# Optimization experiments

Measured on AMD Instinct MI355X. Metric: run time of the kernel, lower is better.

Reference implementation:

```python
import jax, jax.numpy as jnp
import numpy as np

B, T, E, H, V, O = 64, 1024, 256, 512, 32000, 32000


def setup_inputs() -> dict:
    key = jax.random.key(0)
    k1, k2, k3, k4 = jax.random.split(key, 4)
    initrange = 0.1
    x = jax.random.randint(k1, (B, T), 0, V)
    hidden = jnp.zeros((B, H), dtype=jnp.float32)
    emb_table = jax.random.uniform(k2, (V, E), jnp.float32, -initrange, initrange)
    W_i2h = jax.random.uniform(k3, (H, E + H), jnp.float32, -initrange, initrange)
    b_i2h = jnp.zeros((H,), jnp.float32)
    W_dec = jax.random.uniform(k4, (O, H), jnp.float32, -initrange, initrange)
    b_dec = jnp.zeros((O,), jnp.float32)
    return {"x": x, "hidden": hidden, "emb_table": emb_table,
            "W_i2h": W_i2h, "b_i2h": b_i2h, "W_dec": W_dec, "b_dec": b_dec}


def reference(x, hidden, emb_table, W_i2h, b_i2h, W_dec, b_dec):
    # padding_idx=0: row 0 contributes zeros
    tab = emb_table.at[0].set(0.0)
    x_emb = tab[x]                       # [B, T, E]
    xs = jnp.swapaxes(x_emb, 0, 1)       # [T, B, E] for scan over time

    def step(hid, emb):
        combined = jnp.concatenate((hid, emb), axis=1)        # [B, H+E]
        hid = jnp.tanh(combined @ W_i2h.T + b_i2h)            # [B, H]
        return hid, None

    hidden, _ = jax.lax.scan(step, hidden, xs)
    output = hidden @ W_dec.T + b_dec                         # [B, O]
    return output, hidden
```

## Files before the change

### kernel.cpp

```cpp
#include <hip/hip_runtime.h>
#include <math.h>

#define BB 64
#define TT 1024
#define EE 256
#define HH 512
#define OO 32000
#define KDIM 768

typedef float f32x2 __attribute__((ext_vector_type(2)));
typedef unsigned long long u64;

__device__ __forceinline__ f32x2 mk2(float a, float b) { f32x2 r; r.x = a; r.y = b; return r; }

#if __has_builtin(__builtin_elementwise_fma)
#define FMA2(a, b, c) __builtin_elementwise_fma((a), (b), (c))
#else
__device__ __forceinline__ f32x2 FMA2(f32x2 a, f32x2 b, f32x2 c) {
  c.x = fmaf(a.x, b.x, c.x); c.y = fmaf(a.y, b.y, c.y); return c;
}
#endif

__device__ __forceinline__ float fast_tanh(float x) {
  float xc = fminf(fmaxf(x, -10.0f), 10.0f);
  float e;
  asm("v_exp_f32 %0, %1" : "=v"(e) : "v"(xc * 2.885390081777927f));
  float r;
  asm("v_rcp_f32 %0, %1" : "=v"(r) : "v"(e + 1.0f));
  return (e - 1.0f) * r;
}

__device__ __forceinline__ u64 ldw(const u64* p) {
  return __hip_atomic_load(p, __ATOMIC_RELAXED, __HIP_MEMORY_SCOPE_AGENT);
}

#define FORQ(M, J) M(J,0) M(J,1) M(J,2) M(J,3) M(J,4) M(J,5)
#define FORALL(M) FORQ(M,0) FORQ(M,1) FORQ(M,2) FORQ(M,3)

#define WLOAD(J,Q) float4 v##J##_##Q = wr##J[gi##Q]; \
  f32x2 wa##J##_##Q = mk2(v##J##_##Q.x, v##J##_##Q.y); \
  f32x2 wb##J##_##Q = mk2(v##J##_##Q.z, v##J##_##Q.w);
#define WPIN(J,Q) asm volatile("" : "+v"(wa##J##_##Q), "+v"(wb##J##_##Q));
#define WFMA(J,Q) acc##J = FMA2(wa##J##_##Q, mk2(cc##Q.x, cc##Q.y), acc##J); \
                  acc##J = FMA2(wb##J##_##Q, mk2(cc##Q.z, cc##Q.w), acc##J);
#define CHUNK1(J) WFMA(J,0) WFMA(J,1) WFMA(J,2)
#define CHUNK2(J) WFMA(J,3) WFMA(J,4) WFMA(J,5)

__global__ __launch_bounds__(1024, 4) void rnn_kernel(
    const int* __restrict__ x, const float* __restrict__ hidden0,
    const float* __restrict__ emb, const float* __restrict__ Wi,
    const float* __restrict__ bi, float* __restrict__ hid_out,
    u64* __restrict__ psum)
{
  __shared__ float4 comb4[256];
  __shared__ float4 part4[32 * 32];
  __shared__ float part2[128];
  __shared__ int xrow[TT];
  float* comb = (float*)comb4;
  float* part = (float*)part4;

  const int bid = blockIdx.x;
  const int b = bid & 63, s = bid >> 6;
  const int tid = threadIdx.x;
  const int jo = tid & 31;
  const int kg = tid >> 5;
  const bool isLocal = (tid < 512);

  xrow[tid] = x[b * TT + tid];

  if (tid < HH) {
    int j = tid;
    float v = hidden0[b * HH + j];
    int addr = ((j >> 7) == s) ? (j - 128 * s)
                               : (640 + (j < 128 * s ? j : j - 128));
    comb[addr] = v;
  }
  if (tid >= 896 && tid < 960) {
    int t = tid - 896;
    int idx = x[b * TT];
    float4 e0 = make_float4(0.f, 0.f, 0.f, 0.f);
    if (idx != 0) e0 = ((const float4*)emb)[idx * (EE / 4) + t];
    comb4[32 + t] = e0;
  }

  const int c4b = 6 * (isLocal ? kg : (kg - 16));
  const int t32s = 32 * s;
  const int c4_0 = c4b + 0, c4_1 = c4b + 1, c4_2 = c4b + 2;
  const int c4_3 = c4b + 3, c4_4 = c4b + 4, c4_5 = c4b + 5;
  const int gi0 = isLocal ? (c4_0 < 32 ? t32s + c4_0 : 96 + c4_0) : (c4_0 + (c4_0 >= t32s ? 32 : 0));
  const int gi1 = isLocal ? (c4_1 < 32 ? t32s + c4_1 : 96 + c4_1) : (c4_1 + (c4_1 >= t32s ? 32 : 0));
  const int gi2 = isLocal ? (c4_2 < 32 ? t32s + c4_2 : 96 + c4_2) : (c4_2 + (c4_2 >= t32s ? 32 : 0));
  const int gi3 = isLocal ? (c4_3 < 32 ? t32s + c4_3 : 96 + c4_3) : (c4_3 + (c4_3 >= t32s ? 32 : 0));
  const int gi4 = isLocal ? (c4_4 < 32 ? t32s + c4_4 : 96 + c4_4) : (c4_4 + (c4_4 >= t32s ? 32 : 0));
  const int gi5 = isLocal ? (c4_5 < 32 ? t32s + c4_5 : 96 + c4_5) : (c4_5 + (c4_5 >= t32s ? 32 : 0));
  const float4* Wi4 = (const float4*)Wi;
  const float4* wr0 = Wi4 + (size_t)(s * 128 + jo * 4 + 0) * (KDIM / 4);
  const float4* wr1 = wr0 + (KDIM / 4);
  const float4* wr2 = wr1 + (KDIM / 4);
  const float4* wr3 = wr2 + (KDIM / 4);
  FORALL(WLOAD)
  FORALL(WPIN)
  const float bias = (tid < 128) ? bi[s * 128 + tid] : 0.0f;
  __syncthreads();

  const int last = TT - 1;

  #pragma unroll 1
  for (int i = 0; i < TT; ++i) {
    const int ebuf = i & 1;
    if (isLocal) {
      const int eo = ebuf * 64;
      const int a0 = c4_0 + (c4_0 >= 32 ? eo : 0);
      const int a1 = c4_1 + (c4_1 >= 32 ? eo : 0);
      const int a2 = c4_2 + (c4_2 >= 32 ? eo : 0);
      const int a3 = c4_3 + (c4_3 >= 32 ? eo : 0);
      const int a4 = c4_4 + (c4_4 >= 32 ? eo : 0);
      const int a5 = c4_5 + (c4_5 >= 32 ? eo : 0);
      f32x2 acc0 = mk2(0.f, 0.f), acc1 = mk2(0.f, 0.f);
      f32x2 acc2 = mk2(0.f, 0.f), acc3 = mk2(0.f, 0.f);
      {
        float4 cc0 = comb4[a0], cc1 = comb4[a1], cc2 = comb4[a2];
        CHUNK1(0) CHUNK1(1) CHUNK1(2) CHUNK1(3)
        float4 cc3 = comb4[a3], cc4 = comb4[a4], cc5 = comb4[a5];
        CHUNK2(0) CHUNK2(1) CHUNK2(2) CHUNK2(3)
      }
      part4[kg * 32 + jo] = make_float4(acc0.x + acc0.y, acc1.x + acc1.y,
                                        acc2.x + acc2.y, acc3.x + acc3.y);
    } else {
      const int r = tid - 512;
      if (r < 384) {
        if (i > 0) {
          const int fj = r + (r >= 128 * s ? 128 : 0);
          const u64* pw = psum + (size_t)(ebuf * BB + b) * HH + fj;
          const unsigned tgt = (unsigned)i;
          u64 v = ldw(pw);
          while ((unsigned)(v >> 32) < tgt) v = ldw(pw);
          comb[640 + r] = __uint_as_float((unsigned)v);
        }
      } else if (r < 448 && i != last) {
        int t = r - 384;
        int idx = xrow[i + 1];
        float4 e4 = make_float4(0.f, 0.f, 0.f, 0.f);
        if (idx != 0) e4 = ((const float4*)emb)[idx * (EE / 4) + t];
        comb4[32 + (ebuf ^ 1) * 64 + t] = e4;
      }
    }
    __syncthreads();

    if (!isLocal) {
      f32x2 acc0 = mk2(0.f, 0.f), acc1 = mk2(0.f, 0.f);
      f32x2 acc2 = mk2(0.f, 0.f), acc3 = mk2(0.f, 0.f);
      {
        float4 cc0 = comb4[160 + c4_0], cc1 = comb4[160 + c4_1], cc2 = comb4[160 + c4_2];
        CHUNK1(0) CHUNK1(1) CHUNK1(2) CHUNK1(3)
        float4 cc3 = comb4[160 + c4_3], cc4 = comb4[160 + c4_4], cc5 = comb4[160 + c4_5];
        CHUNK2(0) CHUNK2(1) CHUNK2(2) CHUNK2(3)
      }
      part4[kg * 32 + jo] = make_float4(acc0.x + acc0.y, acc1.x + acc1.y,
                                        acc2.x + acc2.y, acc3.x + acc3.y);
    } else if (tid < 128) {
      float ssum = part[0 * 128 + tid] + part[1 * 128 + tid]
                 + part[2 * 128 + tid] + part[3 * 128 + tid]
                 + part[4 * 128 + tid] + part[5 * 128 + tid]
                 + part[6 * 128 + tid] + part[7 * 128 + tid]
                 + part[8 * 128 + tid] + part[9 * 128 + tid]
                 + part[10 * 128 + tid] + part[11 * 128 + tid]
                 + part[12 * 128 + tid] + part[13 * 128 + tid]
                 + part[14 * 128 + tid] + part[15 * 128 + tid];
      part2[tid] = ssum;
    }
    __syncthreads();

    if (tid < 128) {
      float ssum = bias + part2[tid]
                 + part[16 * 128 + tid] + part[17 * 128 + tid]
                 + part[18 * 128 + tid] + part[19 * 128 + tid]
                 + part[20 * 128 + tid] + part[21 * 128 + tid]
                 + part[22 * 128 + tid] + part[23 * 128 + tid]
                 + part[24 * 128 + tid] + part[25 * 128 + tid]
                 + part[26 * 128 + tid] + part[27 * 128 + tid]
                 + part[28 * 128 + tid] + part[29 * 128 + tid]
                 + part[30 * 128 + tid] + part[31 * 128 + tid];
      float h = fast_tanh(ssum);
      if (i == last) {
        hid_out[b * HH + s * 128 + tid] = h;
      } else {
        comb[tid] = h;
        u64 pv = ((u64)(unsigned)(i + 1) << 32) | __float_as_uint(h);
        __hip_atomic_store(psum + (size_t)(((i + 1) & 1) * BB + b) * HH
                               + (s * 128 + tid),
                           pv, __ATOMIC_RELAXED, __HIP_MEMORY_SCOPE_AGENT);
      }
    }
    __syncthreads();
  }
}

__global__ __launch_bounds__(256) void dec_kernel(
    const float* __restrict__ hid, const float* __restrict__ Wd,
    const float* __restrict__ bd, float* __restrict__ out)
{
  __shared__ float4 hl4[32 * 128];
  const int o  = blockIdx.x * 256 + threadIdx.x;
  const int b0 = blockIdx.y * 32;

  const float4* hid4 = (const float4*)(hid + b0 * HH);
  #pragma unroll
  for (int i = 0; i < 16; ++i) {
    int lin = i * 256 + threadIdx.x;
    hl4[lin] = hid4[lin];
  }
  __syncthreads();

  f32x2 acc[32];
  #pragma unroll
  for (int bb = 0; bb < 32; ++bb) acc[bb] = mk2(0.f, 0.f);

  const float4* W4 = (const float4*)(Wd + (size_t)o * HH);
  for (int j4 = 0; j4 < 128; ++j4) {
    float4 w = W4[j4];
    f32x2 wa = mk2(w.x, w.y), wb = mk2(w.z, w.w);
    #pragma unroll
    for (int bb = 0; bb < 32; ++bb) {
      float4 h = hl4[bb * 128 + j4];
      acc[bb] = FMA2(wa, mk2(h.x, h.y), acc[bb]);
      acc[bb] = FMA2(wb, mk2(h.z, h.w), acc[bb]);
    }
  }

  const float bias = bd[o];
  #pragma unroll
  for (int bb = 0; bb < 32; ++bb)
    out[(size_t)(b0 + bb) * OO + o] = acc[bb].x + acc[bb].y + bias;
}

extern "C" void kernel_launch(void* const* d_in, const int* in_sizes, int n_in,
                              void* d_out, int out_size, void* d_ws, size_t ws_size,
                              hipStream_t stream) {
  const int*   x    = (const int*)  d_in[0];
  const float* hid0 = (const float*)d_in[1];
  const float* emb  = (const float*)d_in[2];
  const float* Wi   = (const float*)d_in[3];
  const float* bi   = (const float*)d_in[4];
  const float* Wd   = (const float*)d_in[5];
  const float* bd   = (const float*)d_in[6];

  float* out     = (float*)d_out;
  float* hid_out = out + (size_t)BB * OO;

  u64* psum = (u64*)d_ws;

  hipMemsetAsync(d_ws, 0, (size_t)2 * BB * HH * sizeof(u64), stream);

  rnn_kernel<<<BB * 4, 1024, 0, stream>>>(x, hid0, emb, Wi, bi, hid_out, psum);
  dec_kernel<<<dim3(OO / 256, BB / 32), 256, 0, stream>>>(hid_out, Wd, bd, out);
}
```

Baseline: 1.341 ms.

## Use workgroup-scope L2 atomics for cross-block exchange when all four blocks share an XCC

Each block reads its XCC ID at start-up, and the four blocks serving one batch row check whether they landed on the same XCC and can see each other's tokens through workgroup-scope CAS. If every check passes, the per-step hidden-state exchange switches to workgroup-scope stores and CAS-based polling. These stay in the shared L2 instead of going out to agent-scope coherence, which is meant to cut inter-block synchronisation latency on the 1024-step serial chain. It adds a start-up handshake and relies on hardware scheduling and memory-model behaviour that is not guaranteed. When the blocks do not share an XCC it falls back to the old path.

```diff
diff --git a/kernel.cpp b/kernel.cpp
--- a/kernel.cpp
+++ b/kernel.cpp
@@ -32,6 +32,23 @@
 
 __device__ __forceinline__ u64 ldw(const u64* p) {
   return __hip_atomic_load(p, __ATOMIC_RELAXED, __HIP_MEMORY_SCOPE_AGENT);
+}
+__device__ __forceinline__ unsigned lda32(const unsigned* p) {
+  return __hip_atomic_load(p, __ATOMIC_RELAXED, __HIP_MEMORY_SCOPE_AGENT);
+}
+__device__ __forceinline__ u64 cas_l2(u64* p) {
+  u64 exp = 0xFFFFFFFFFFFFFFFFull;
+  __hip_atomic_compare_exchange_strong(p, &exp, 0xFFFFFFFFFFFFFFFFull,
+                                       __ATOMIC_RELAXED, __ATOMIC_RELAXED,
+                                       __HIP_MEMORY_SCOPE_WORKGROUP);
+  return exp;
+}
+__device__ __forceinline__ unsigned cas32_l2(unsigned* p) {
+  unsigned exp = 0xDEADBEEFu;
+  __hip_atomic_compare_exchange_strong(p, &exp, 0xDEADBEEFu,
+                                       __ATOMIC_RELAXED, __ATOMIC_RELAXED,
+                                       __HIP_MEMORY_SCOPE_WORKGROUP);
+  return exp;
 }
 
 #define FORQ(M, J) M(J,0) M(J,1) M(J,2) M(J,3) M(J,4) M(J,5)
@@ -50,12 +67,13 @@
     const int* __restrict__ x, const float* __restrict__ hidden0,
     const float* __restrict__ emb, const float* __restrict__ Wi,
     const float* __restrict__ bi, float* __restrict__ hid_out,
-    u64* __restrict__ psum)
+    u64* __restrict__ psum, unsigned* __restrict__ ctrl)
 {
   __shared__ float4 comb4[256];
   __shared__ float4 part4[32 * 32];
   __shared__ float part2[128];
   __shared__ int xrow[TT];
+  __shared__ unsigned fastmode_s;
   float* comb = (float*)comb4;
   float* part = (float*)part4;
 
@@ -81,6 +99,46 @@
     float4 e0 = make_float4(0.f, 0.f, 0.f, 0.f);
     if (idx != 0) e0 = ((const float4*)emb)[idx * (EE / 4) + t];
     comb4[32 + t] = e0;
+  }
+
+  if (tid == 0) {
+    unsigned* chk  = ctrl;
+    unsigned* tok  = ctrl + 256;
+    unsigned* verd = ctrl + 512;
+    unsigned myx;
+    asm volatile("s_getreg_b32 %0, hwreg(HW_REG_XCC_ID)" : "=s"(myx));
+    __hip_atomic_store(&chk[bid], myx + 1u, __ATOMIC_RELAXED,
+                       __HIP_MEMORY_SCOPE_AGENT);
+    unsigned v0, v1, v2, v3;
+    do {
+      v0 = lda32(&chk[b +   0]); v1 = lda32(&chk[b +  64]);
+      v2 = lda32(&chk[b + 128]); v3 = lda32(&chk[b + 192]);
+      if (!(v0 && v1 && v2 && v3)) __builtin_amdgcn_s_sleep(8);
+    } while (!(v0 && v1 && v2 && v3));
+    unsigned myverd = 2u;
+    if (v0 == v1 && v1 == v2 && v2 == v3) {
+      __hip_atomic_store(&tok[bid], 1u, __ATOMIC_RELAXED,
+                         __HIP_MEMORY_SCOPE_WORKGROUP);
+      unsigned* t0 = &tok[b + 64 * ((s + 1) & 3)];
+      unsigned* t1 = &tok[b + 64 * ((s + 2) & 3)];
+      unsigned* t2 = &tok[b + 64 * ((s + 3) & 3)];
+      int ok = 0;
+      for (int it = 0; it < 16384 && ok != 7; ++it) {
+        if (!(ok & 1) && cas32_l2(t0) != 0u) ok |= 1;
+        if (!(ok & 2) && cas32_l2(t1) != 0u) ok |= 2;
+        if (!(ok & 4) && cas32_l2(t2) != 0u) ok |= 4;
+      }
+      if (ok == 7) myverd = 1u;
+    }
+    __hip_atomic_store(&verd[bid], myverd, __ATOMIC_RELAXED,
+                       __HIP_MEMORY_SCOPE_AGENT);
+    unsigned w0, w1, w2, w3;
+    do {
+      w0 = lda32(&verd[b +   0]); w1 = lda32(&verd[b +  64]);
+      w2 = lda32(&verd[b + 128]); w3 = lda32(&verd[b + 192]);
+      if (!(w0 && w1 && w2 && w3)) __builtin_amdgcn_s_sleep(8);
+    } while (!(w0 && w1 && w2 && w3));
+    fastmode_s = (w0 == 1u && w1 == 1u && w2 == 1u && w3 == 1u) ? 1u : 0u;
   }
 
   const int c4b = 6 * (isLocal ? kg : (kg - 16));
@@ -103,6 +161,7 @@
   const float bias = (tid < 128) ? bi[s * 128 + tid] : 0.0f;
   __syncthreads();
 
+  const bool fastm = (fastmode_s != 0u);
   const int last = TT - 1;
 
   #pragma unroll 1
@@ -131,10 +190,11 @@
       if (r < 384) {
         if (i > 0) {
           const int fj = r + (r >= 128 * s ? 128 : 0);
-          const u64* pw = psum + (size_t)(ebuf * BB + b) * HH + fj;
+          u64* pw = psum + (size_t)(ebuf * BB + b) * HH + fj;
           const unsigned tgt = (unsigned)i;
-          u64 v = ldw(pw);
-          while ((unsigned)(v >> 32) < tgt) v = ldw(pw);
+          u64 v;
+          if (fastm) { do { v = cas_l2(pw); } while ((unsigned)(v >> 32) < tgt); }
+          else       { do { v = ldw(pw);    } while ((unsigned)(v >> 32) < tgt); }
           comb[640 + r] = __uint_as_float((unsigned)v);
         }
       } else if (r < 448 && i != last) {
@@ -187,9 +247,13 @@
       } else {
         comb[tid] = h;
         u64 pv = ((u64)(unsigned)(i + 1) << 32) | __float_as_uint(h);
-        __hip_atomic_store(psum + (size_t)(((i + 1) & 1) * BB + b) * HH
-                               + (s * 128 + tid),
-                           pv, __ATOMIC_RELAXED, __HIP_MEMORY_SCOPE_AGENT);
+        u64* pp = psum + (size_t)(((i + 1) & 1) * BB + b) * HH + (s * 128 + tid);
+        if (fastm)
+          __hip_atomic_store(pp, pv, __ATOMIC_RELAXED,
+                             __HIP_MEMORY_SCOPE_WORKGROUP);
+        else
+          __hip_atomic_store(pp, pv, __ATOMIC_RELAXED,
+                             __HIP_MEMORY_SCOPE_AGENT);
       }
     }
     __syncthreads();
@@ -248,10 +312,12 @@
   float* out     = (float*)d_out;
   float* hid_out = out + (size_t)BB * OO;
 
-  u64* psum = (u64*)d_ws;
-
-  hipMemsetAsync(d_ws, 0, (size_t)2 * BB * HH * sizeof(u64), stream);
-
-  rnn_kernel<<<BB * 4, 1024, 0, stream>>>(x, hid0, emb, Wi, bi, hid_out, psum);
+  unsigned* ctrl = (unsigned*)d_ws;
+  u64* psum = (u64*)((char*)d_ws + 16384);
+
+  hipMemsetAsync(d_ws, 0, 16384 + (size_t)2 * BB * HH * sizeof(u64), stream);
+
+  rnn_kernel<<<BB * 4, 1024, 0, stream>>>(x, hid0, emb, Wi, bi, hid_out,
+                                          psum, ctrl);
   dec_kernel<<<dim3(OO / 256, BB / 32), 256, 0, stream>>>(hid_out, Wd, bd, out);
 }
```

New measurement: 1.648 ms. 1.23x slower.

## Process two batch rows per block and interleave their recurrence phases

Applied to the files above, without the earlier changes.

Each block now handles two batch rows (A and B) sharing the same register-resident weight slice, halving the grid to 128 blocks. The per-step schedule is staggered so that the cross-block spin-wait for one row overlaps with the local matvec and reduction of the other row. The goal is to hide inter-block synchronization latency and reuse the pinned weights across two rows. In exchange, each block does twice the FMA work per step and uses more shared memory, with fewer blocks in flight.

```diff
diff --git a/kernel.cpp b/kernel.cpp
--- a/kernel.cpp
+++ b/kernel.cpp
@@ -46,41 +46,62 @@
 #define CHUNK1(J) WFMA(J,0) WFMA(J,1) WFMA(J,2)
 #define CHUNK2(J) WFMA(J,3) WFMA(J,4) WFMA(J,5)
 
+#define FMA96(A0, A1, A2, A3, A4, A5, DST) { \
+  f32x2 acc0 = mk2(0.f,0.f), acc1 = mk2(0.f,0.f); \
+  f32x2 acc2 = mk2(0.f,0.f), acc3 = mk2(0.f,0.f); \
+  float4 cc0 = comb4[A0], cc1 = comb4[A1], cc2 = comb4[A2]; \
+  CHUNK1(0) CHUNK1(1) CHUNK1(2) CHUNK1(3) \
+  float4 cc3 = comb4[A3], cc4 = comb4[A4], cc5 = comb4[A5]; \
+  CHUNK2(0) CHUNK2(1) CHUNK2(2) CHUNK2(3) \
+  DST = make_float4(acc0.x + acc0.y, acc1.x + acc1.y, \
+                    acc2.x + acc2.y, acc3.x + acc3.y); }
+
 __global__ __launch_bounds__(1024, 4) void rnn_kernel(
     const int* __restrict__ x, const float* __restrict__ hidden0,
     const float* __restrict__ emb, const float* __restrict__ Wi,
     const float* __restrict__ bi, float* __restrict__ hid_out,
     u64* __restrict__ psum)
 {
-  __shared__ float4 comb4[256];
-  __shared__ float4 part4[32 * 32];
+  __shared__ float4 comb4[512];
+  __shared__ float4 part4A[32 * 32];
+  __shared__ float4 part4B[32 * 32];
   __shared__ float part2[128];
-  __shared__ int xrow[TT];
-  float* comb = (float*)comb4;
-  float* part = (float*)part4;
+  __shared__ int xrowA[TT], xrowB[TT];
+  float* comb  = (float*)comb4;
+  float* partA = (float*)part4A;
+  float* partB = (float*)part4B;
 
   const int bid = blockIdx.x;
-  const int b = bid & 63, s = bid >> 6;
+  const int p = bid & 31, s = bid >> 5;
+  const int rA = 2 * p, rB = 2 * p + 1;
   const int tid = threadIdx.x;
   const int jo = tid & 31;
   const int kg = tid >> 5;
   const bool isLocal = (tid < 512);
 
-  xrow[tid] = x[b * TT + tid];
-
-  if (tid < HH) {
-    int j = tid;
-    float v = hidden0[b * HH + j];
-    int addr = ((j >> 7) == s) ? (j - 128 * s)
-                               : (640 + (j < 128 * s ? j : j - 128));
+  xrowA[tid] = x[rA * TT + tid];
+  xrowB[tid] = x[rB * TT + tid];
+
+  {
+    const int j = tid & 511;
+    const int row = isLocal ? rA : rB;
+    float v = hidden0[row * HH + j];
+    int addr;
+    if ((j >> 7) == s) addr = (isLocal ? 0 : 128) + (j - 128 * s);
+    else {
+      int r = (j < 128 * s) ? j : (j - 128);
+      addr = (isLocal ? 1280 : 1664) + r;
+    }
     comb[addr] = v;
   }
-  if (tid >= 896 && tid < 960) {
+  if (tid >= 896) {
     int t = tid - 896;
-    int idx = x[b * TT];
+    int row = (t < 64) ? rA : rB;
+    int tt = t & 63;
+    int idx = x[row * TT];
     float4 e0 = make_float4(0.f, 0.f, 0.f, 0.f);
-    if (idx != 0) e0 = ((const float4*)emb)[idx * (EE / 4) + t];
-    comb4[32 + t] = e0;
+    if (idx != 0) e0 = ((const float4*)emb)[idx * (EE / 4) + tt];
+    comb4[(t < 64 ? 64 : 192) + tt] = e0;
   }
 
   const int c4b = 6 * (isLocal ? kg : (kg - 16));
@@ -104,92 +125,108 @@
   __syncthreads();
 
   const int last = TT - 1;
+  const int pr = tid - 512;
+  const int fj = (pr >= 0 && pr < 384) ? (pr + (pr >= 128 * s ? 128 : 0)) : 0;
 
   #pragma unroll 1
   for (int i = 0; i < TT; ++i) {
     const int ebuf = i & 1;
+    const int nbuf = ebuf ^ 1;
+    const unsigned tgt = (unsigned)i;
+    u64* pbaseR = psum + (size_t)(ebuf * BB) * HH;
+    u64* pbaseW = psum + (size_t)(nbuf * BB) * HH;
+
     if (isLocal) {
-      const int eo = ebuf * 64;
-      const int a0 = c4_0 + (c4_0 >= 32 ? eo : 0);
-      const int a1 = c4_1 + (c4_1 >= 32 ? eo : 0);
-      const int a2 = c4_2 + (c4_2 >= 32 ? eo : 0);
-      const int a3 = c4_3 + (c4_3 >= 32 ? eo : 0);
-      const int a4 = c4_4 + (c4_4 >= 32 ? eo : 0);
-      const int a5 = c4_5 + (c4_5 >= 32 ? eo : 0);
-      f32x2 acc0 = mk2(0.f, 0.f), acc1 = mk2(0.f, 0.f);
-      f32x2 acc2 = mk2(0.f, 0.f), acc3 = mk2(0.f, 0.f);
-      {
-        float4 cc0 = comb4[a0], cc1 = comb4[a1], cc2 = comb4[a2];
-        CHUNK1(0) CHUNK1(1) CHUNK1(2) CHUNK1(3)
-        float4 cc3 = comb4[a3], cc4 = comb4[a4], cc5 = comb4[a5];
-        CHUNK2(0) CHUNK2(1) CHUNK2(2) CHUNK2(3)
+      const int eoA = 32 + ebuf * 64;
+      FMA96(c4_0 + (c4_0 < 32 ? 0 : eoA), c4_1 + (c4_1 < 32 ? 0 : eoA),
+            c4_2 + (c4_2 < 32 ? 0 : eoA), c4_3 + (c4_3 < 32 ? 0 : eoA),
+            c4_4 + (c4_4 < 32 ? 0 : eoA), c4_5 + (c4_5 < 32 ? 0 : eoA),
+            part4A[kg * 32 + jo])
+    } else if (pr < 384) {
+      if (i > 0) {
+        const u64* pw = pbaseR + (size_t)rB * HH + fj;
+        u64 v = ldw(pw);
+        while ((unsigned)(v >> 32) < tgt) v = ldw(pw);
+        comb[1664 + pr] = __uint_as_float((unsigned)v);
       }
-      part4[kg * 32 + jo] = make_float4(acc0.x + acc0.y, acc1.x + acc1.y,
-                                        acc2.x + acc2.y, acc3.x + acc3.y);
+    } else if (i != last) {
+      int t = tid - 896;
+      int row = (t < 64) ? rA : rB;
+      int tt = t & 63;
+      int idx = (t < 64) ? xrowA[i + 1] : xrowB[i + 1];
+      float4 e4 = make_float4(0.f, 0.f, 0.f, 0.f);
+      if (idx != 0) e4 = ((const float4*)emb)[idx * (EE / 4) + tt];
+      comb4[(t < 64 ? 64 : 192) + nbuf * 64 + tt] = e4;
+    }
+    __syncthreads();
+
+    if (isLocal) {
+      const int eoB = 160 + ebuf * 64;
+      FMA96(c4_0 + (c4_0 < 32 ? 32 : eoB), c4_1 + (c4_1 < 32 ? 32 : eoB),
+            c4_2 + (c4_2 < 32 ? 32 : eoB), c4_3 + (c4_3 < 32 ? 32 : eoB),
+            c4_4 + (c4_4 < 32 ? 32 : eoB), c4_5 + (c4_5 < 32 ? 32 : eoB),
+            part4B[kg * 32 + jo])
     } else {
-      const int r = tid - 512;
-      if (r < 384) {
-        if (i > 0) {
-          const int fj = r + (r >= 128 * s ? 128 : 0);
-          const u64* pw = psum + (size_t)(ebuf * BB + b) * HH + fj;
-          const unsigned tgt = (unsigned)i;
-          u64 v = ldw(pw);
-          while ((unsigned)(v >> 32) < tgt) v = ldw(pw);
-          comb[640 + r] = __uint_as_float((unsigned)v);
-        }
-      } else if (r < 448 && i != last) {
-        int t = r - 384;
-        int idx = xrow[i + 1];
-        float4 e4 = make_float4(0.f, 0.f, 0.f, 0.f);
-        if (idx != 0) e4 = ((const float4*)emb)[idx * (EE / 4) + t];
-        comb4[32 + (ebuf ^ 1) * 64 + t] = e4;
+      FMA96(416 + c4_0, 416 + c4_1, 416 + c4_2,
+            416 + c4_3, 416 + c4_4, 416 + c4_5,
+            part4B[kg * 32 + jo])
+    }
+    __syncthreads();
+
+    if (tid < 128) {
+      float ssum = bias
+        + partB[ 0*128+tid] + partB[ 1*128+tid] + partB[ 2*128+tid] + partB[ 3*128+tid]
+        + partB[ 4*128+tid] + partB[ 5*128+tid] + partB[ 6*128+tid] + partB[ 7*128+tid]
+        + partB[ 8*128+tid] + partB[ 9*128+tid] + partB[10*128+tid] + partB[11*128+tid]
+        + partB[12*128+tid] + partB[13*128+tid] + partB[14*128+tid] + partB[15*128+tid]
+        + partB[16*128+tid] + partB[17*128+tid] + partB[18*128+tid] + partB[19*128+tid]
+        + partB[20*128+tid] + partB[21*128+tid] + partB[22*128+tid] + partB[23*128+tid]
+        + partB[24*128+tid] + partB[25*128+tid] + partB[26*128+tid] + partB[27*128+tid]
+        + partB[28*128+tid] + partB[29*128+tid] + partB[30*128+tid] + partB[31*128+tid];
+      float h = fast_tanh(ssum);
+      if (i == last) {
+        hid_out[rB * HH + s * 128 + tid] = h;
+      } else {
+        comb[128 + tid] = h;
+        u64 pv = ((u64)(unsigned)(i + 1) << 32) | __float_as_uint(h);
+        __hip_atomic_store(pbaseW + (size_t)rB * HH + (s * 128 + tid), pv,
+                           __ATOMIC_RELAXED, __HIP_MEMORY_SCOPE_AGENT);
       }
+    } else if (pr >= 0 && pr < 384 && i > 0) {
+      const u64* pw = pbaseR + (size_t)rA * HH + fj;
+      u64 v = ldw(pw);
+      while ((unsigned)(v >> 32) < tgt) v = ldw(pw);
+      comb[1280 + pr] = __uint_as_float((unsigned)v);
     }
     __syncthreads();
 
     if (!isLocal) {
-      f32x2 acc0 = mk2(0.f, 0.f), acc1 = mk2(0.f, 0.f);
-      f32x2 acc2 = mk2(0.f, 0.f), acc3 = mk2(0.f, 0.f);
-      {
-        float4 cc0 = comb4[160 + c4_0], cc1 = comb4[160 + c4_1], cc2 = comb4[160 + c4_2];
-        CHUNK1(0) CHUNK1(1) CHUNK1(2) CHUNK1(3)
-        float4 cc3 = comb4[160 + c4_3], cc4 = comb4[160 + c4_4], cc5 = comb4[160 + c4_5];
-        CHUNK2(0) CHUNK2(1) CHUNK2(2) CHUNK2(3)
-      }
-      part4[kg * 32 + jo] = make_float4(acc0.x + acc0.y, acc1.x + acc1.y,
-                                        acc2.x + acc2.y, acc3.x + acc3.y);
+      FMA96(320 + c4_0, 320 + c4_1, 320 + c4_2,
+            320 + c4_3, 320 + c4_4, 320 + c4_5,
+            part4A[kg * 32 + jo])
     } else if (tid < 128) {
-      float ssum = part[0 * 128 + tid] + part[1 * 128 + tid]
-                 + part[2 * 128 + tid] + part[3 * 128 + tid]
-                 + part[4 * 128 + tid] + part[5 * 128 + tid]
-                 + part[6 * 128 + tid] + part[7 * 128 + tid]
-                 + part[8 * 128 + tid] + part[9 * 128 + tid]
-                 + part[10 * 128 + tid] + part[11 * 128 + tid]
-                 + part[12 * 128 + tid] + part[13 * 128 + tid]
-                 + part[14 * 128 + tid] + part[15 * 128 + tid];
-      part2[tid] = ssum;
+      part2[tid] =
+          partA[ 0*128+tid] + partA[ 1*128+tid] + partA[ 2*128+tid] + partA[ 3*128+tid]
+        + partA[ 4*128+tid] + partA[ 5*128+tid] + partA[ 6*128+tid] + partA[ 7*128+tid]
+        + partA[ 8*128+tid] + partA[ 9*128+tid] + partA[10*128+tid] + partA[11*128+tid]
+        + partA[12*128+tid] + partA[13*128+tid] + partA[14*128+tid] + partA[15*128+tid];
     }
     __syncthreads();
 
     if (tid < 128) {
       float ssum = bias + part2[tid]
-                 + part[16 * 128 + tid] + part[17 * 128 + tid]
-                 + part[18 * 128 + tid] + part[19 * 128 + tid]
-                 + part[20 * 128 + tid] + part[21 * 128 + tid]
-                 + part[22 * 128 + tid] + part[23 * 128 + tid]
-                 + part[24 * 128 + tid] + part[25 * 128 + tid]
-                 + part[26 * 128 + tid] + part[27 * 128 + tid]
-                 + part[28 * 128 + tid] + part[29 * 128 + tid]
-                 + part[30 * 128 + tid] + part[31 * 128 + tid];
+        + partA[16*128+tid] + partA[17*128+tid] + partA[18*128+tid] + partA[19*128+tid]
+        + partA[20*128+tid] + partA[21*128+tid] + partA[22*128+tid] + partA[23*128+tid]
+        + partA[24*128+tid] + partA[25*128+tid] + partA[26*128+tid] + partA[27*128+tid]
+        + partA[28*128+tid] + partA[29*128+tid] + partA[30*128+tid] + partA[31*128+tid];
       float h = fast_tanh(ssum);
       if (i == last) {
-        hid_out[b * HH + s * 128 + tid] = h;
+        hid_out[rA * HH + s * 128 + tid] = h;
       } else {
         comb[tid] = h;
         u64 pv = ((u64)(unsigned)(i + 1) << 32) | __float_as_uint(h);
-        __hip_atomic_store(psum + (size_t)(((i + 1) & 1) * BB + b) * HH
-                               + (s * 128 + tid),
-                           pv, __ATOMIC_RELAXED, __HIP_MEMORY_SCOPE_AGENT);
+        __hip_atomic_store(pbaseW + (size_t)rA * HH + (s * 128 + tid), pv,
+                           __ATOMIC_RELAXED, __HIP_MEMORY_SCOPE_AGENT);
       }
     }
     __syncthreads();
@@ -252,6 +289,6 @@
 
   hipMemsetAsync(d_ws, 0, (size_t)2 * BB * HH * sizeof(u64), stream);
 
-  rnn_kernel<<<BB * 4, 1024, 0, stream>>>(x, hid0, emb, Wi, bi, hid_out, psum);
+  rnn_kernel<<<BB / 2 * 4, 1024, 0, stream>>>(x, hid0, emb, Wi, bi, hid_out, psum);
   dec_kernel<<<dim3(OO / 256, BB / 32), 256, 0, stream>>>(hid_out, Wd, bd, out);
 }
```

Measured after the change: 3.284 ms. 145% more time.
